# Optimization experiments

Hardware: AMD Instinct MI355X
Metric: run time of the kernel (lower is better)

## Reference

```python
import jax, jax.numpy as jnp
import numpy as np

N = 100000   # nodes
E = 600000   # edges
D_IN, D_H, D_OUT = 128, 128, 128


def glorot(key, shape):
    lim = float(np.sqrt(6.0 / (shape[0] + shape[1])))
    return jax.random.uniform(key, shape, jnp.float32, -lim, lim)


def setup_inputs() -> dict:
    key = jax.random.key(0)
    k1, k2, k3, k4 = jax.random.split(key, 4)
    x = jax.random.normal(k1, (N, D_IN), jnp.float32)
    edge_index = jax.random.randint(k2, (2, E), 0, N, jnp.int64)
    W1 = glorot(k3, (D_IN, D_H))
    b1 = jnp.zeros((D_H,), jnp.float32)
    W2 = glorot(k4, (D_H, D_OUT))
    b2 = jnp.zeros((D_OUT,), jnp.float32)
    return {"x": x, "W1": W1, "b1": b1, "W2": W2, "b2": b2, "edge_index": edge_index}


def gcn_conv(x, W, b, src, dst, n):
    # GCNConv: D^{-1/2}(A+I)D^{-1/2} X W + b  (self loops already in src/dst)
    h = x @ W                                   # [N, d_out]
    ones = jnp.ones(src.shape[0], h.dtype)
    deg = jax.ops.segment_sum(ones, dst, num_segments=n)      # in-degree incl self loop
    dinv = jnp.where(deg > 0, jax.lax.rsqrt(deg), 0.0)        # deg^{-1/2}
    norm = dinv[src] * dinv[dst]                              # [E+N]
    msgs = h[src] * norm[:, None]                             # gather + scale
    out = jax.ops.segment_sum(msgs, dst, num_segments=n)      # scatter-add to targets
    return out + b


def reference(x, W1, b1, W2, b2, edge_index):
    loop = jnp.arange(N, dtype=edge_index.dtype)
    src = jnp.concatenate([edge_index[0], loop])
    dst = jnp.concatenate([edge_index[1], loop])
    h = gcn_conv(x, W1, b1, src, dst, N)
    h = jax.nn.relu(h)  # dropout is a no-op in eval mode
    return gcn_conv(h, W2, b2, src, dst, N)
```

## Files before the change

kernel.cpp:

```cpp
#include <hip/hip_runtime.h>

#define NFEAT 128

typedef __attribute__((ext_vector_type(8))) short bf16x8;
typedef __attribute__((ext_vector_type(4))) float f32x4;

__device__ inline ushort f2b(float v) {
  unsigned u = __builtin_bit_cast(unsigned, v);
  return (ushort)((u + 0x7FFFu + ((u >> 16) & 1u)) >> 16);
}


__global__ __launch_bounds__(256) void k_hist(const int* __restrict__ dst,
                                              int* __restrict__ cnt, int E, int N) {
  int range = blockIdx.x & 7, chunk = blockIdx.x >> 3;
  int lo = (int)(((long long)range * N) >> 3);
  int hi = (int)(((long long)(range + 1) * N) >> 3);
  int i = chunk * 1024 + threadIdx.x * 4;
  if (i + 3 < E) {
    int4 d4 = *(const int4*)(dst + i);
    if ((unsigned)(d4.x - lo) < (unsigned)(hi - lo)) atomicAdd(&cnt[d4.x], 1);
    if ((unsigned)(d4.y - lo) < (unsigned)(hi - lo)) atomicAdd(&cnt[d4.y], 1);
    if ((unsigned)(d4.z - lo) < (unsigned)(hi - lo)) atomicAdd(&cnt[d4.z], 1);
    if ((unsigned)(d4.w - lo) < (unsigned)(hi - lo)) atomicAdd(&cnt[d4.w], 1);
  } else {
    for (int j = 0; j < 4; j++) {
      if (i + j < E) {
        int d = dst[i + j];
        if ((unsigned)(d - lo) < (unsigned)(hi - lo)) atomicAdd(&cnt[d], 1);
      }
    }
  }
}

__global__ __launch_bounds__(256) void k_scan_blocks(const int* __restrict__ cnt,
                                                     int* __restrict__ rowptr,
                                                     int* __restrict__ bsum,
                                                     float* __restrict__ dinv, int n) {
  __shared__ int s[256];
  int tid = threadIdx.x;
  int idx = blockIdx.x * 1024 + tid * 4;
  int v[4];
  int sum = 0;
#pragma unroll
  for (int j = 0; j < 4; j++) {
    int c = 0;
    if (idx + j < n) {
      c = cnt[idx + j];
      dinv[idx + j] = rsqrtf((float)(c + 1));
    }
    v[j] = (idx + j < n) ? ((c + 8) & ~7) : 0;
    sum += v[j];
  }
  s[tid] = sum;
  __syncthreads();
  for (int off = 1; off < 256; off <<= 1) {
    int t = (tid >= off) ? s[tid - off] : 0;
    __syncthreads();
    s[tid] += t;
    __syncthreads();
  }
  if (tid == 255) bsum[blockIdx.x] = s[255];
  int run = s[tid] - sum;
#pragma unroll
  for (int j = 0; j < 4; j++) {
    if (idx + j < n) rowptr[idx + j] = run;
    run += v[j];
  }
}

__global__ __launch_bounds__(256) void k_scan_addcur(int* __restrict__ rowptr,
                                                     const int* __restrict__ bsum,
                                                     int* __restrict__ cursor,
                                                     const float* __restrict__ dinv,
                                                     int2* __restrict__ csr2,
                                                     int n, int nb) {
  __shared__ int s[256];
  int tid = threadIdx.x;
  int v = (tid < nb) ? bsum[tid] : 0;
  s[tid] = v;
  __syncthreads();
  for (int off = 1; off < 256; off <<= 1) {
    int t = (tid >= off) ? s[tid - off] : 0;
    __syncthreads();
    s[tid] += t;
    __syncthreads();
  }
  int total = s[255];
  __syncthreads();
  int ex = s[tid] - v;
  __syncthreads();
  s[tid] = ex;
  __syncthreads();
  int i = blockIdx.x * 256 + tid;
  if (i < n) {
    int rp = rowptr[i] + s[i >> 10];
    rowptr[i] = rp;
    cursor[i] = rp + 1;
    int2 self;
    self.x = i;
    self.y = __float_as_int(dinv[i]);
    csr2[rp] = self;
  }
  if (i == 0) rowptr[n] = total;
}

__global__ __launch_bounds__(256) void k_scatter(const int* __restrict__ src,
                                                 const int* __restrict__ dst,
                                                 const float* __restrict__ dinv,
                                                 int* __restrict__ cursor,
                                                 int2* __restrict__ csr2, int E, int N) {
  int range = blockIdx.x & 7, chunk = blockIdx.x >> 3;
  int lo = (int)(((long long)range * N) >> 3);
  int hi = (int)(((long long)(range + 1) * N) >> 3);
  int i = chunk * 1024 + threadIdx.x * 4;
  if (i + 3 < E) {
    int4 d4 = *(const int4*)(dst + i);
    int4 s4 = *(const int4*)(src + i);
    int dd[4] = {d4.x, d4.y, d4.z, d4.w};
    int ss[4] = {s4.x, s4.y, s4.z, s4.w};
#pragma unroll
    for (int j = 0; j < 4; j++) {
      if ((unsigned)(dd[j] - lo) < (unsigned)(hi - lo)) {
        int p = atomicAdd(&cursor[dd[j]], 1);
        int2 v;
        v.x = ss[j];
        v.y = __float_as_int(dinv[ss[j]]);
        csr2[p] = v;
      }
    }
  } else {
    for (int j = 0; j < 4; j++) {
      if (i + j < E) {
        int d = dst[i + j];
        if ((unsigned)(d - lo) < (unsigned)(hi - lo)) {
          int s = src[i + j];
          int p = atomicAdd(&cursor[d], 1);
          int2 v;
          v.x = s;
          v.y = __float_as_int(dinv[s]);
          csr2[p] = v;
        }
      }
    }
  }
}

__global__ __launch_bounds__(256) void k_cast_w(const float* __restrict__ W1,
                                                const float* __restrict__ W2,
                                                ushort* __restrict__ WT1,
                                                ushort* __restrict__ WT2) {
  int b = blockIdx.x;
  const float* W = (b < 64) ? W1 : W2;
  ushort* WT = (b < 64) ? WT1 : WT2;
  int idx = (b & 63) * 256 + threadIdx.x;
  int k = idx >> 7, nn = idx & 127;
  WT[nn * 128 + k] = f2b(W[idx]);
}


template <bool AFP32>
__global__ __launch_bounds__(256) void k_gemm(const void* __restrict__ Av,
                                              const ushort* __restrict__ WT,
                                              ushort* __restrict__ out, int n) {
  __shared__ ushort sW[128][136];
  int tid = threadIdx.x;
  {
    int r = tid >> 1, hh = tid & 1;
    const uint4* srcp = (const uint4*)(WT + r * 128 + hh * 64);
    uint4* dstp = (uint4*)(&sW[r][hh * 64]);
#pragma unroll
    for (int j = 0; j < 8; j++) dstp[j] = srcp[j];
  }
  __syncthreads();

  int wave = tid >> 6;
  int lane = tid & 63;
  int l16 = lane & 15;
  int quad = lane >> 4;
  int rowBase = blockIdx.x * 128 + wave * 32;

  bf16x8 afrag[2][4];
#pragma unroll
  for (int rt = 0; rt < 2; rt++) {
    int row = rowBase + rt * 16 + l16;
    row = min(row, n - 1);
    if (AFP32) {
      const float* Ap = (const float*)Av + (size_t)row * NFEAT + quad * 8;
#pragma unroll
      for (int ks = 0; ks < 4; ks++) {
        float4 f0 = *(const float4*)(Ap + ks * 32);
        float4 f1 = *(const float4*)(Ap + ks * 32 + 4);
        ushort t[8] = {f2b(f0.x), f2b(f0.y), f2b(f0.z), f2b(f0.w),
                       f2b(f1.x), f2b(f1.y), f2b(f1.z), f2b(f1.w)};
        afrag[rt][ks] = *(const bf16x8*)t;
      }
    } else {
      const ushort* Ap = (const ushort*)Av + (size_t)row * NFEAT + quad * 8;
#pragma unroll
      for (int ks = 0; ks < 4; ks++) afrag[rt][ks] = *(const bf16x8*)(Ap + ks * 32);
    }
  }

#pragma unroll
  for (int ct = 0; ct < 8; ct++) {
    bf16x8 bfrag[4];
#pragma unroll
    for (int ks = 0; ks < 4; ks++)
      bfrag[ks] = *(const bf16x8*)(&sW[ct * 16 + l16][ks * 32 + quad * 8]);
    f32x4 acc[2] = {{0.f, 0.f, 0.f, 0.f}, {0.f, 0.f, 0.f, 0.f}};
#pragma unroll
    for (int rt = 0; rt < 2; rt++)
#pragma unroll
      for (int ks = 0; ks < 4; ks++)
        acc[rt] = __builtin_amdgcn_mfma_f32_16x16x32_bf16(afrag[rt][ks], bfrag[ks],
                                                          acc[rt], 0, 0, 0);
#pragma unroll
    for (int rt = 0; rt < 2; rt++)
#pragma unroll
      for (int r = 0; r < 4; r++) {
        int row = rowBase + rt * 16 + quad * 4 + r;
        if (row < n) out[(size_t)row * NFEAT + ct * 16 + l16] = f2b(acc[rt][r]);
      }
  }
}


__global__ __launch_bounds__(256) void k_agg(const ushort* __restrict__ h,
                                             const float* __restrict__ dinv,
                                             const int* __restrict__ rowptr,
                                             const int2* __restrict__ csr2,
                                             const float* __restrict__ bias,
                                             ushort* __restrict__ out_bf,
                                             float* __restrict__ out_f32,
                                             int n, int relu_bf) {
  int node = blockIdx.x * 8 + (threadIdx.x >> 5);
  if (node >= n) return;
  int c = (threadIdx.x & 31) * 4;
  float a0 = 0.f, a1 = 0.f, a2 = 0.f, a3 = 0.f;

  int e = rowptr[node], end = rowptr[node + 1];
  for (; e < end; e += 8) {
    int4 q0 = *(const int4*)(csr2 + e);
    int4 q1 = *(const int4*)(csr2 + e + 2);
    int4 q2 = *(const int4*)(csr2 + e + 4);
    int4 q3 = *(const int4*)(csr2 + e + 6);
    uint2 h0 = *(const uint2*)(h + (size_t)q0.x * NFEAT + c);
    uint2 h1 = *(const uint2*)(h + (size_t)q0.z * NFEAT + c);
    uint2 h2 = *(const uint2*)(h + (size_t)q1.x * NFEAT + c);
    uint2 h3 = *(const uint2*)(h + (size_t)q1.z * NFEAT + c);
    uint2 h4 = *(const uint2*)(h + (size_t)q2.x * NFEAT + c);
    uint2 h5 = *(const uint2*)(h + (size_t)q2.z * NFEAT + c);
    uint2 h6 = *(const uint2*)(h + (size_t)q3.x * NFEAT + c);
    uint2 h7 = *(const uint2*)(h + (size_t)q3.z * NFEAT + c);
    float w0 = __int_as_float(q0.y), w1 = __int_as_float(q0.w);
    float w2 = __int_as_float(q1.y), w3 = __int_as_float(q1.w);
    float w4 = __int_as_float(q2.y), w5 = __int_as_float(q2.w);
    float w6 = __int_as_float(q3.y), w7 = __int_as_float(q3.w);
    a0 = fmaf(w0, __uint_as_float(h0.x << 16), a0);
    a1 = fmaf(w0, __uint_as_float(h0.x & 0xffff0000u), a1);
    a2 = fmaf(w0, __uint_as_float(h0.y << 16), a2);
    a3 = fmaf(w0, __uint_as_float(h0.y & 0xffff0000u), a3);
    a0 = fmaf(w1, __uint_as_float(h1.x << 16), a0);
    a1 = fmaf(w1, __uint_as_float(h1.x & 0xffff0000u), a1);
    a2 = fmaf(w1, __uint_as_float(h1.y << 16), a2);
    a3 = fmaf(w1, __uint_as_float(h1.y & 0xffff0000u), a3);
    a0 = fmaf(w2, __uint_as_float(h2.x << 16), a0);
    a1 = fmaf(w2, __uint_as_float(h2.x & 0xffff0000u), a1);
    a2 = fmaf(w2, __uint_as_float(h2.y << 16), a2);
    a3 = fmaf(w2, __uint_as_float(h2.y & 0xffff0000u), a3);
    a0 = fmaf(w3, __uint_as_float(h3.x << 16), a0);
    a1 = fmaf(w3, __uint_as_float(h3.x & 0xffff0000u), a1);
    a2 = fmaf(w3, __uint_as_float(h3.y << 16), a2);
    a3 = fmaf(w3, __uint_as_float(h3.y & 0xffff0000u), a3);
    a0 = fmaf(w4, __uint_as_float(h4.x << 16), a0);
    a1 = fmaf(w4, __uint_as_float(h4.x & 0xffff0000u), a1);
    a2 = fmaf(w4, __uint_as_float(h4.y << 16), a2);
    a3 = fmaf(w4, __uint_as_float(h4.y & 0xffff0000u), a3);
    a0 = fmaf(w5, __uint_as_float(h5.x << 16), a0);
    a1 = fmaf(w5, __uint_as_float(h5.x & 0xffff0000u), a1);
    a2 = fmaf(w5, __uint_as_float(h5.y << 16), a2);
    a3 = fmaf(w5, __uint_as_float(h5.y & 0xffff0000u), a3);
    a0 = fmaf(w6, __uint_as_float(h6.x << 16), a0);
    a1 = fmaf(w6, __uint_as_float(h6.x & 0xffff0000u), a1);
    a2 = fmaf(w6, __uint_as_float(h6.y << 16), a2);
    a3 = fmaf(w6, __uint_as_float(h6.y & 0xffff0000u), a3);
    a0 = fmaf(w7, __uint_as_float(h7.x << 16), a0);
    a1 = fmaf(w7, __uint_as_float(h7.x & 0xffff0000u), a1);
    a2 = fmaf(w7, __uint_as_float(h7.y << 16), a2);
    a3 = fmaf(w7, __uint_as_float(h7.y & 0xffff0000u), a3);
  }

  float di = dinv[node];
  float4 b = *(const float4*)(bias + c);
  float o0 = fmaf(di, a0, b.x);
  float o1 = fmaf(di, a1, b.y);
  float o2 = fmaf(di, a2, b.z);
  float o3 = fmaf(di, a3, b.w);
  if (relu_bf) {
    o0 = fmaxf(o0, 0.f); o1 = fmaxf(o1, 0.f);
    o2 = fmaxf(o2, 0.f); o3 = fmaxf(o3, 0.f);
    uint2 pk;
    pk.x = f2b(o0) | ((unsigned)f2b(o1) << 16);
    pk.y = f2b(o2) | ((unsigned)f2b(o3) << 16);
    *(uint2*)(out_bf + (size_t)node * NFEAT + c) = pk;
  } else {
    float4 o = {o0, o1, o2, o3};
    *(float4*)(out_f32 + (size_t)node * NFEAT + c) = o;
  }
}


extern "C" void kernel_launch(void* const* d_in, const int* in_sizes, int n_in,
                              void* d_out, int out_size, void* d_ws, size_t ws_size,
                              hipStream_t stream) {
  const float* x = (const float*)d_in[0];
  const float* W1 = (const float*)d_in[1];
  const float* b1 = (const float*)d_in[2];
  const float* W2 = (const float*)d_in[3];
  const float* b2 = (const float*)d_in[4];
  const int* ei = (const int*)d_in[5];

  const int N = in_sizes[0] / NFEAT;
  const int E = in_sizes[5] / 2;
  const int* srcIdx = ei;
  const int* dstIdx = ei + E;

  char* p = (char*)d_ws;
  auto alloc = [&](size_t bytes) {
    char* r = p;
    p += (bytes + 255) & ~(size_t)255;
    return r;
  };
  int* cnt = (int*)alloc((size_t)N * 4);
  int2* csr2 = (int2*)alloc((size_t)(E + 8 * N + 16) * 8);
  char* memset_end = p;
  int* cursor = (int*)alloc((size_t)N * 4);
  float* dinv = (float*)alloc((size_t)N * 4);
  int* rowptr = (int*)alloc((size_t)(N + 1) * 4);
  int* bsum = (int*)alloc(1024);
  ushort* WT1 = (ushort*)alloc(NFEAT * NFEAT * 2);
  ushort* WT2 = (ushort*)alloc(NFEAT * NFEAT * 2);
  ushort* t1 = (ushort*)alloc((size_t)N * NFEAT * 2);
  ushort* h2 = (ushort*)alloc((size_t)N * NFEAT * 2);
  ushort* h1 = (ushort*)d_out;
  float* out = (float*)d_out;

  hipMemsetAsync(cnt, 0, (size_t)(memset_end - (char*)cnt), stream);

  int nb = (N + 1023) / 1024;
  int gEx = ((E + 1023) / 1024) * 8;

  k_hist<<<gEx, 256, 0, stream>>>(dstIdx, cnt, E, N);
  k_scan_blocks<<<nb, 256, 0, stream>>>(cnt, rowptr, bsum, dinv, N);
  k_scan_addcur<<<(N + 255) / 256, 256, 0, stream>>>(rowptr, bsum, cursor, dinv, csr2,
                                                     N, nb);
  k_scatter<<<gEx, 256, 0, stream>>>(srcIdx, dstIdx, dinv, cursor, csr2, E, N);
  k_cast_w<<<128, 256, 0, stream>>>(W1, W2, WT1, WT2);

  int gG = (N + 127) / 128;
  int gA = (N + 7) / 8;

  k_gemm<true><<<gG, 256, 0, stream>>>(x, WT1, h1, N);
  k_agg<<<gA, 256, 0, stream>>>(h1, dinv, rowptr, csr2, b1, t1, nullptr, N, 1);
  k_gemm<false><<<gG, 256, 0, stream>>>(t1, WT2, h2, N);
  k_agg<<<gA, 256, 0, stream>>>(h2, dinv, rowptr, csr2, b2, nullptr, out, N, 0);
}
```

Measured before the change: 265.9 us.

## Fuse layer-1 aggregation with layer-2 GEMM and overlap histogram with first GEMM

Several restructurings land together. The first GEMM and the in-degree histogram now run as one launch, with blocks split between the two roles. The first-layer aggregation (with bias and ReLU) is fused with the second GEMM through shared memory, so the t1 intermediate is no longer written to and read back from global memory. CSR row padding drops from 8 to 4, with the gather loop unrolled 4-wide to match, and scan_addcur blocks are remapped by node range, probably for locality with the scatter partitioning. The risks are less memory-level parallelism in the gather loop, and lower occupancy in the fused kernel from its larger shared-memory footprint and serial per-block aggregation batches.

```diff
diff --git a/kernel.cpp b/kernel.cpp
--- a/kernel.cpp
+++ b/kernel.cpp
@@ -10,253 +10,18 @@
   return (ushort)((u + 0x7FFFu + ((u >> 16) & 1u)) >> 16);
 }
 
-
-__global__ __launch_bounds__(256) void k_hist(const int* __restrict__ dst,
-                                              int* __restrict__ cnt, int E, int N) {
-  int range = blockIdx.x & 7, chunk = blockIdx.x >> 3;
-  int lo = (int)(((long long)range * N) >> 3);
-  int hi = (int)(((long long)(range + 1) * N) >> 3);
-  int i = chunk * 1024 + threadIdx.x * 4;
-  if (i + 3 < E) {
-    int4 d4 = *(const int4*)(dst + i);
-    if ((unsigned)(d4.x - lo) < (unsigned)(hi - lo)) atomicAdd(&cnt[d4.x], 1);
-    if ((unsigned)(d4.y - lo) < (unsigned)(hi - lo)) atomicAdd(&cnt[d4.y], 1);
-    if ((unsigned)(d4.z - lo) < (unsigned)(hi - lo)) atomicAdd(&cnt[d4.z], 1);
-    if ((unsigned)(d4.w - lo) < (unsigned)(hi - lo)) atomicAdd(&cnt[d4.w], 1);
-  } else {
-    for (int j = 0; j < 4; j++) {
-      if (i + j < E) {
-        int d = dst[i + j];
-        if ((unsigned)(d - lo) < (unsigned)(hi - lo)) atomicAdd(&cnt[d], 1);
-      }
-    }
-  }
-}
-
-__global__ __launch_bounds__(256) void k_scan_blocks(const int* __restrict__ cnt,
-                                                     int* __restrict__ rowptr,
-                                                     int* __restrict__ bsum,
-                                                     float* __restrict__ dinv, int n) {
-  __shared__ int s[256];
-  int tid = threadIdx.x;
-  int idx = blockIdx.x * 1024 + tid * 4;
-  int v[4];
-  int sum = 0;
-#pragma unroll
-  for (int j = 0; j < 4; j++) {
-    int c = 0;
-    if (idx + j < n) {
-      c = cnt[idx + j];
-      dinv[idx + j] = rsqrtf((float)(c + 1));
-    }
-    v[j] = (idx + j < n) ? ((c + 8) & ~7) : 0;
-    sum += v[j];
-  }
-  s[tid] = sum;
-  __syncthreads();
-  for (int off = 1; off < 256; off <<= 1) {
-    int t = (tid >= off) ? s[tid - off] : 0;
-    __syncthreads();
-    s[tid] += t;
-    __syncthreads();
-  }
-  if (tid == 255) bsum[blockIdx.x] = s[255];
-  int run = s[tid] - sum;
-#pragma unroll
-  for (int j = 0; j < 4; j++) {
-    if (idx + j < n) rowptr[idx + j] = run;
-    run += v[j];
-  }
-}
-
-__global__ __launch_bounds__(256) void k_scan_addcur(int* __restrict__ rowptr,
-                                                     const int* __restrict__ bsum,
-                                                     int* __restrict__ cursor,
-                                                     const float* __restrict__ dinv,
-                                                     int2* __restrict__ csr2,
-                                                     int n, int nb) {
-  __shared__ int s[256];
-  int tid = threadIdx.x;
-  int v = (tid < nb) ? bsum[tid] : 0;
-  s[tid] = v;
-  __syncthreads();
-  for (int off = 1; off < 256; off <<= 1) {
-    int t = (tid >= off) ? s[tid - off] : 0;
-    __syncthreads();
-    s[tid] += t;
-    __syncthreads();
-  }
-  int total = s[255];
-  __syncthreads();
-  int ex = s[tid] - v;
-  __syncthreads();
-  s[tid] = ex;
-  __syncthreads();
-  int i = blockIdx.x * 256 + tid;
-  if (i < n) {
-    int rp = rowptr[i] + s[i >> 10];
-    rowptr[i] = rp;
-    cursor[i] = rp + 1;
-    int2 self;
-    self.x = i;
-    self.y = __float_as_int(dinv[i]);
-    csr2[rp] = self;
-  }
-  if (i == 0) rowptr[n] = total;
-}
-
-__global__ __launch_bounds__(256) void k_scatter(const int* __restrict__ src,
-                                                 const int* __restrict__ dst,
-                                                 const float* __restrict__ dinv,
-                                                 int* __restrict__ cursor,
-                                                 int2* __restrict__ csr2, int E, int N) {
-  int range = blockIdx.x & 7, chunk = blockIdx.x >> 3;
-  int lo = (int)(((long long)range * N) >> 3);
-  int hi = (int)(((long long)(range + 1) * N) >> 3);
-  int i = chunk * 1024 + threadIdx.x * 4;
-  if (i + 3 < E) {
-    int4 d4 = *(const int4*)(dst + i);
-    int4 s4 = *(const int4*)(src + i);
-    int dd[4] = {d4.x, d4.y, d4.z, d4.w};
-    int ss[4] = {s4.x, s4.y, s4.z, s4.w};
-#pragma unroll
-    for (int j = 0; j < 4; j++) {
-      if ((unsigned)(dd[j] - lo) < (unsigned)(hi - lo)) {
-        int p = atomicAdd(&cursor[dd[j]], 1);
-        int2 v;
-        v.x = ss[j];
-        v.y = __float_as_int(dinv[ss[j]]);
-        csr2[p] = v;
-      }
-    }
-  } else {
-    for (int j = 0; j < 4; j++) {
-      if (i + j < E) {
-        int d = dst[i + j];
-        if ((unsigned)(d - lo) < (unsigned)(hi - lo)) {
-          int s = src[i + j];
-          int p = atomicAdd(&cursor[d], 1);
-          int2 v;
-          v.x = s;
-          v.y = __float_as_int(dinv[s]);
-          csr2[p] = v;
-        }
-      }
-    }
-  }
-}
-
-__global__ __launch_bounds__(256) void k_cast_w(const float* __restrict__ W1,
-                                                const float* __restrict__ W2,
-                                                ushort* __restrict__ WT1,
-                                                ushort* __restrict__ WT2) {
-  int b = blockIdx.x;
-  const float* W = (b < 64) ? W1 : W2;
-  ushort* WT = (b < 64) ? WT1 : WT2;
-  int idx = (b & 63) * 256 + threadIdx.x;
-  int k = idx >> 7, nn = idx & 127;
-  WT[nn * 128 + k] = f2b(W[idx]);
-}
-
-
-template <bool AFP32>
-__global__ __launch_bounds__(256) void k_gemm(const void* __restrict__ Av,
-                                              const ushort* __restrict__ WT,
-                                              ushort* __restrict__ out, int n) {
-  __shared__ ushort sW[128][136];
-  int tid = threadIdx.x;
-  {
-    int r = tid >> 1, hh = tid & 1;
-    const uint4* srcp = (const uint4*)(WT + r * 128 + hh * 64);
-    uint4* dstp = (uint4*)(&sW[r][hh * 64]);
-#pragma unroll
-    for (int j = 0; j < 8; j++) dstp[j] = srcp[j];
-  }
-  __syncthreads();
-
-  int wave = tid >> 6;
-  int lane = tid & 63;
-  int l16 = lane & 15;
-  int quad = lane >> 4;
-  int rowBase = blockIdx.x * 128 + wave * 32;
-
-  bf16x8 afrag[2][4];
-#pragma unroll
-  for (int rt = 0; rt < 2; rt++) {
-    int row = rowBase + rt * 16 + l16;
-    row = min(row, n - 1);
-    if (AFP32) {
-      const float* Ap = (const float*)Av + (size_t)row * NFEAT + quad * 8;
-#pragma unroll
-      for (int ks = 0; ks < 4; ks++) {
-        float4 f0 = *(const float4*)(Ap + ks * 32);
-        float4 f1 = *(const float4*)(Ap + ks * 32 + 4);
-        ushort t[8] = {f2b(f0.x), f2b(f0.y), f2b(f0.z), f2b(f0.w),
-                       f2b(f1.x), f2b(f1.y), f2b(f1.z), f2b(f1.w)};
-        afrag[rt][ks] = *(const bf16x8*)t;
-      }
-    } else {
-      const ushort* Ap = (const ushort*)Av + (size_t)row * NFEAT + quad * 8;
-#pragma unroll
-      for (int ks = 0; ks < 4; ks++) afrag[rt][ks] = *(const bf16x8*)(Ap + ks * 32);
-    }
-  }
-
-#pragma unroll
-  for (int ct = 0; ct < 8; ct++) {
-    bf16x8 bfrag[4];
-#pragma unroll
-    for (int ks = 0; ks < 4; ks++)
-      bfrag[ks] = *(const bf16x8*)(&sW[ct * 16 + l16][ks * 32 + quad * 8]);
-    f32x4 acc[2] = {{0.f, 0.f, 0.f, 0.f}, {0.f, 0.f, 0.f, 0.f}};
-#pragma unroll
-    for (int rt = 0; rt < 2; rt++)
-#pragma unroll
-      for (int ks = 0; ks < 4; ks++)
-        acc[rt] = __builtin_amdgcn_mfma_f32_16x16x32_bf16(afrag[rt][ks], bfrag[ks],
-                                                          acc[rt], 0, 0, 0);
-#pragma unroll
-    for (int rt = 0; rt < 2; rt++)
-#pragma unroll
-      for (int r = 0; r < 4; r++) {
-        int row = rowBase + rt * 16 + quad * 4 + r;
-        if (row < n) out[(size_t)row * NFEAT + ct * 16 + l16] = f2b(acc[rt][r]);
-      }
-  }
-}
-
-
-__global__ __launch_bounds__(256) void k_agg(const ushort* __restrict__ h,
-                                             const float* __restrict__ dinv,
-                                             const int* __restrict__ rowptr,
-                                             const int2* __restrict__ csr2,
-                                             const float* __restrict__ bias,
-                                             ushort* __restrict__ out_bf,
-                                             float* __restrict__ out_f32,
-                                             int n, int relu_bf) {
-  int node = blockIdx.x * 8 + (threadIdx.x >> 5);
-  if (node >= n) return;
-  int c = (threadIdx.x & 31) * 4;
-  float a0 = 0.f, a1 = 0.f, a2 = 0.f, a3 = 0.f;
-
-  int e = rowptr[node], end = rowptr[node + 1];
-  for (; e < end; e += 8) {
+__device__ inline void agg_accum(const ushort* __restrict__ h,
+                                 const int2* __restrict__ csr2, int e, int end, int c,
+                                 float& a0, float& a1, float& a2, float& a3) {
+  for (; e < end; e += 4) {
     int4 q0 = *(const int4*)(csr2 + e);
     int4 q1 = *(const int4*)(csr2 + e + 2);
-    int4 q2 = *(const int4*)(csr2 + e + 4);
-    int4 q3 = *(const int4*)(csr2 + e + 6);
     uint2 h0 = *(const uint2*)(h + (size_t)q0.x * NFEAT + c);
     uint2 h1 = *(const uint2*)(h + (size_t)q0.z * NFEAT + c);
     uint2 h2 = *(const uint2*)(h + (size_t)q1.x * NFEAT + c);
     uint2 h3 = *(const uint2*)(h + (size_t)q1.z * NFEAT + c);
-    uint2 h4 = *(const uint2*)(h + (size_t)q2.x * NFEAT + c);
-    uint2 h5 = *(const uint2*)(h + (size_t)q2.z * NFEAT + c);
-    uint2 h6 = *(const uint2*)(h + (size_t)q3.x * NFEAT + c);
-    uint2 h7 = *(const uint2*)(h + (size_t)q3.z * NFEAT + c);
     float w0 = __int_as_float(q0.y), w1 = __int_as_float(q0.w);
     float w2 = __int_as_float(q1.y), w3 = __int_as_float(q1.w);
-    float w4 = __int_as_float(q2.y), w5 = __int_as_float(q2.w);
-    float w6 = __int_as_float(q3.y), w7 = __int_as_float(q3.w);
     a0 = fmaf(w0, __uint_as_float(h0.x << 16), a0);
     a1 = fmaf(w0, __uint_as_float(h0.x & 0xffff0000u), a1);
     a2 = fmaf(w0, __uint_as_float(h0.y << 16), a2);
@@ -273,41 +38,311 @@
     a1 = fmaf(w3, __uint_as_float(h3.x & 0xffff0000u), a1);
     a2 = fmaf(w3, __uint_as_float(h3.y << 16), a2);
     a3 = fmaf(w3, __uint_as_float(h3.y & 0xffff0000u), a3);
-    a0 = fmaf(w4, __uint_as_float(h4.x << 16), a0);
-    a1 = fmaf(w4, __uint_as_float(h4.x & 0xffff0000u), a1);
-    a2 = fmaf(w4, __uint_as_float(h4.y << 16), a2);
-    a3 = fmaf(w4, __uint_as_float(h4.y & 0xffff0000u), a3);
-    a0 = fmaf(w5, __uint_as_float(h5.x << 16), a0);
-    a1 = fmaf(w5, __uint_as_float(h5.x & 0xffff0000u), a1);
-    a2 = fmaf(w5, __uint_as_float(h5.y << 16), a2);
-    a3 = fmaf(w5, __uint_as_float(h5.y & 0xffff0000u), a3);
-    a0 = fmaf(w6, __uint_as_float(h6.x << 16), a0);
-    a1 = fmaf(w6, __uint_as_float(h6.x & 0xffff0000u), a1);
-    a2 = fmaf(w6, __uint_as_float(h6.y << 16), a2);
-    a3 = fmaf(w6, __uint_as_float(h6.y & 0xffff0000u), a3);
-    a0 = fmaf(w7, __uint_as_float(h7.x << 16), a0);
-    a1 = fmaf(w7, __uint_as_float(h7.x & 0xffff0000u), a1);
-    a2 = fmaf(w7, __uint_as_float(h7.y << 16), a2);
-    a3 = fmaf(w7, __uint_as_float(h7.y & 0xffff0000u), a3);
-  }
-
+  }
+}
+
+__global__ __launch_bounds__(256) void k_cast_w(const float* __restrict__ W1,
+                                                const float* __restrict__ W2,
+                                                ushort* __restrict__ WT1,
+                                                ushort* __restrict__ WT2) {
+  int b = blockIdx.x;
+  const float* W = (b < 64) ? W1 : W2;
+  ushort* WT = (b < 64) ? WT1 : WT2;
+  int idx = (b & 63) * 256 + threadIdx.x;
+  int k = idx >> 7, nn = idx & 127;
+  WT[nn * 128 + k] = f2b(W[idx]);
+}
+
+
+__global__ __launch_bounds__(256) void k_par1(const float* __restrict__ x,
+                                              const ushort* __restrict__ WT1,
+                                              ushort* __restrict__ h1, int n,
+                                              const int* __restrict__ dst,
+                                              int* __restrict__ cnt, int E,
+                                              int gemmBlocks) {
+  if ((int)blockIdx.x >= gemmBlocks) {
+    int bid = blockIdx.x - gemmBlocks;
+    int range = bid & 7, chunk = bid >> 3;
+    int lo = (int)(((long long)range * n) >> 3);
+    int hi = (int)(((long long)(range + 1) * n) >> 3);
+    int i = chunk * 1024 + threadIdx.x * 4;
+    if (i + 3 < E) {
+      int4 d4 = *(const int4*)(dst + i);
+      if ((unsigned)(d4.x - lo) < (unsigned)(hi - lo)) atomicAdd(&cnt[d4.x], 1);
+      if ((unsigned)(d4.y - lo) < (unsigned)(hi - lo)) atomicAdd(&cnt[d4.y], 1);
+      if ((unsigned)(d4.z - lo) < (unsigned)(hi - lo)) atomicAdd(&cnt[d4.z], 1);
+      if ((unsigned)(d4.w - lo) < (unsigned)(hi - lo)) atomicAdd(&cnt[d4.w], 1);
+    } else {
+      for (int j = 0; j < 4; j++) {
+        if (i + j < E) {
+          int d = dst[i + j];
+          if ((unsigned)(d - lo) < (unsigned)(hi - lo)) atomicAdd(&cnt[d], 1);
+        }
+      }
+    }
+    return;
+  }
+  __shared__ ushort sW[128][136];
+  int tid = threadIdx.x;
+  {
+    int r = tid >> 1, hh = tid & 1;
+    const uint4* srcp = (const uint4*)(WT1 + r * 128 + hh * 64);
+    uint4* dstp = (uint4*)(&sW[r][hh * 64]);
+#pragma unroll
+    for (int j = 0; j < 8; j++) dstp[j] = srcp[j];
+  }
+  __syncthreads();
+
+  int wave = tid >> 6;
+  int lane = tid & 63;
+  int l16 = lane & 15;
+  int quad = lane >> 4;
+  int rowBase = blockIdx.x * 128 + wave * 32;
+
+  bf16x8 afrag[2][4];
+#pragma unroll
+  for (int rt = 0; rt < 2; rt++) {
+    int row = rowBase + rt * 16 + l16;
+    row = min(row, n - 1);
+    const float* Ap = x + (size_t)row * NFEAT + quad * 8;
+#pragma unroll
+    for (int ks = 0; ks < 4; ks++) {
+      float4 f0 = *(const float4*)(Ap + ks * 32);
+      float4 f1 = *(const float4*)(Ap + ks * 32 + 4);
+      ushort t[8] = {f2b(f0.x), f2b(f0.y), f2b(f0.z), f2b(f0.w),
+                     f2b(f1.x), f2b(f1.y), f2b(f1.z), f2b(f1.w)};
+      afrag[rt][ks] = *(const bf16x8*)t;
+    }
+  }
+
+#pragma unroll
+  for (int ct = 0; ct < 8; ct++) {
+    bf16x8 bfrag[4];
+#pragma unroll
+    for (int ks = 0; ks < 4; ks++)
+      bfrag[ks] = *(const bf16x8*)(&sW[ct * 16 + l16][ks * 32 + quad * 8]);
+    f32x4 acc[2] = {{0.f, 0.f, 0.f, 0.f}, {0.f, 0.f, 0.f, 0.f}};
+#pragma unroll
+    for (int rt = 0; rt < 2; rt++)
+#pragma unroll
+      for (int ks = 0; ks < 4; ks++)
+        acc[rt] = __builtin_amdgcn_mfma_f32_16x16x32_bf16(afrag[rt][ks], bfrag[ks],
+                                                          acc[rt], 0, 0, 0);
+#pragma unroll
+    for (int rt = 0; rt < 2; rt++)
+#pragma unroll
+      for (int r = 0; r < 4; r++) {
+        int row = rowBase + rt * 16 + quad * 4 + r;
+        if (row < n) h1[(size_t)row * NFEAT + ct * 16 + l16] = f2b(acc[rt][r]);
+      }
+  }
+}
+
+__global__ __launch_bounds__(256) void k_scan_blocks(const int* __restrict__ cnt,
+                                                     int* __restrict__ rowptr,
+                                                     int* __restrict__ bsum,
+                                                     float* __restrict__ dinv, int n) {
+  __shared__ int s[256];
+  int tid = threadIdx.x;
+  int idx = blockIdx.x * 1024 + tid * 4;
+  int v[4];
+  int sum = 0;
+#pragma unroll
+  for (int j = 0; j < 4; j++) {
+    int c = 0;
+    if (idx + j < n) {
+      c = cnt[idx + j];
+      dinv[idx + j] = rsqrtf((float)(c + 1));
+    }
+    v[j] = (idx + j < n) ? ((c + 4) & ~3) : 0;
+    sum += v[j];
+  }
+  s[tid] = sum;
+  __syncthreads();
+  for (int off = 1; off < 256; off <<= 1) {
+    int t = (tid >= off) ? s[tid - off] : 0;
+    __syncthreads();
+    s[tid] += t;
+    __syncthreads();
+  }
+  if (tid == 255) bsum[blockIdx.x] = s[255];
+  int run = s[tid] - sum;
+#pragma unroll
+  for (int j = 0; j < 4; j++) {
+    if (idx + j < n) rowptr[idx + j] = run;
+    run += v[j];
+  }
+}
+
+__global__ __launch_bounds__(256) void k_scan_addcur(int* __restrict__ rowptr,
+                                                     const int* __restrict__ bsum,
+                                                     int* __restrict__ cursor,
+                                                     const float* __restrict__ dinv,
+                                                     int2* __restrict__ csr2,
+                                                     int n, int nb) {
+  __shared__ int s[256];
+  int tid = threadIdx.x;
+  int v = (tid < nb) ? bsum[tid] : 0;
+  s[tid] = v;
+  __syncthreads();
+  for (int off = 1; off < 256; off <<= 1) {
+    int t = (tid >= off) ? s[tid - off] : 0;
+    __syncthreads();
+    s[tid] += t;
+    __syncthreads();
+  }
+  int total = s[255];
+  __syncthreads();
+  int ex = s[tid] - v;
+  __syncthreads();
+  s[tid] = ex;
+  __syncthreads();
+  int range = blockIdx.x & 7, chunk = blockIdx.x >> 3;
+  int lo = (int)(((long long)range * n) >> 3);
+  int hi = (int)(((long long)(range + 1) * n) >> 3);
+  int i = lo + chunk * 256 + tid;
+  if (i < hi) {
+    int rp = rowptr[i] + s[i >> 10];
+    rowptr[i] = rp;
+    cursor[i] = rp + 1;
+    int2 self;
+    self.x = i;
+    self.y = __float_as_int(dinv[i]);
+    csr2[rp] = self;
+  }
+  if (blockIdx.x == 0 && tid == 0) rowptr[n] = total;
+}
+
+__global__ __launch_bounds__(256) void k_scatter(const int* __restrict__ src,
+                                                 const int* __restrict__ dst,
+                                                 const float* __restrict__ dinv,
+                                                 int* __restrict__ cursor,
+                                                 int2* __restrict__ csr2, int E, int N) {
+  int range = blockIdx.x & 7, chunk = blockIdx.x >> 3;
+  int lo = (int)(((long long)range * N) >> 3);
+  int hi = (int)(((long long)(range + 1) * N) >> 3);
+  int i = chunk * 1024 + threadIdx.x * 4;
+  if (i + 3 < E) {
+    int4 d4 = *(const int4*)(dst + i);
+    int4 s4 = *(const int4*)(src + i);
+    int dd[4] = {d4.x, d4.y, d4.z, d4.w};
+    int ss[4] = {s4.x, s4.y, s4.z, s4.w};
+#pragma unroll
+    for (int j = 0; j < 4; j++) {
+      if ((unsigned)(dd[j] - lo) < (unsigned)(hi - lo)) {
+        int p = atomicAdd(&cursor[dd[j]], 1);
+        int2 v;
+        v.x = ss[j];
+        v.y = __float_as_int(dinv[ss[j]]);
+        csr2[p] = v;
+      }
+    }
+  } else {
+    for (int j = 0; j < 4; j++) {
+      if (i + j < E) {
+        int d = dst[i + j];
+        if ((unsigned)(d - lo) < (unsigned)(hi - lo)) {
+          int s = src[i + j];
+          int p = atomicAdd(&cursor[d], 1);
+          int2 v;
+          v.x = s;
+          v.y = __float_as_int(dinv[s]);
+          csr2[p] = v;
+        }
+      }
+    }
+  }
+}
+
+
+__global__ __launch_bounds__(256) void k_fused(const ushort* __restrict__ h1,
+                                               const float* __restrict__ dinv,
+                                               const int* __restrict__ rowptr,
+                                               const int2* __restrict__ csr2,
+                                               const float* __restrict__ b1,
+                                               const ushort* __restrict__ WT2,
+                                               ushort* __restrict__ h2, int n) {
+  __shared__ ushort sW[128][136];
+  __shared__ ushort sT[64][136];
+  int tid = threadIdx.x;
+  {
+    int r = tid >> 1, hh = tid & 1;
+    const uint4* srcp = (const uint4*)(WT2 + r * 128 + hh * 64);
+    uint4* dstp = (uint4*)(&sW[r][hh * 64]);
+#pragma unroll
+    for (int j = 0; j < 8; j++) dstp[j] = srcp[j];
+  }
+
+  int base = blockIdx.x * 64;
+  int c = (tid & 31) * 4;
+#pragma unroll 1
+  for (int batch = 0; batch < 8; batch++) {
+    int nl = batch * 8 + (tid >> 5);
+    int node = base + nl;
+    if (node < n) {
+      float a0 = 0.f, a1 = 0.f, a2 = 0.f, a3 = 0.f;
+      agg_accum(h1, csr2, rowptr[node], rowptr[node + 1], c, a0, a1, a2, a3);
+      float di = dinv[node];
+      float4 bb = *(const float4*)(b1 + c);
+      float o0 = fmaxf(fmaf(di, a0, bb.x), 0.f);
+      float o1 = fmaxf(fmaf(di, a1, bb.y), 0.f);
+      float o2 = fmaxf(fmaf(di, a2, bb.z), 0.f);
+      float o3 = fmaxf(fmaf(di, a3, bb.w), 0.f);
+      uint2 pk;
+      pk.x = f2b(o0) | ((unsigned)f2b(o1) << 16);
+      pk.y = f2b(o2) | ((unsigned)f2b(o3) << 16);
+      *(uint2*)(&sT[nl][c]) = pk;
+    }
+  }
+  __syncthreads();
+
+  int wave = tid >> 6;
+  int lane = tid & 63;
+  int l16 = lane & 15;
+  int quad = lane >> 4;
+  bf16x8 afrag[4];
+#pragma unroll
+  for (int ks = 0; ks < 4; ks++)
+    afrag[ks] = *(const bf16x8*)(&sT[wave * 16 + l16][ks * 32 + quad * 8]);
+
+#pragma unroll
+  for (int ct = 0; ct < 8; ct++) {
+    bf16x8 bfrag[4];
+#pragma unroll
+    for (int ks = 0; ks < 4; ks++)
+      bfrag[ks] = *(const bf16x8*)(&sW[ct * 16 + l16][ks * 32 + quad * 8]);
+    f32x4 acc = {0.f, 0.f, 0.f, 0.f};
+#pragma unroll
+    for (int ks = 0; ks < 4; ks++)
+      acc = __builtin_amdgcn_mfma_f32_16x16x32_bf16(afrag[ks], bfrag[ks], acc, 0, 0, 0);
+#pragma unroll
+    for (int r = 0; r < 4; r++) {
+      int row = base + wave * 16 + quad * 4 + r;
+      if (row < n) h2[(size_t)row * NFEAT + ct * 16 + l16] = f2b(acc[r]);
+    }
+  }
+}
+
+
+__global__ __launch_bounds__(256) void k_agg2(const ushort* __restrict__ h,
+                                              const float* __restrict__ dinv,
+                                              const int* __restrict__ rowptr,
+                                              const int2* __restrict__ csr2,
+                                              const float* __restrict__ bias,
+                                              float* __restrict__ out, int n) {
+  int node = blockIdx.x * 8 + (threadIdx.x >> 5);
+  if (node >= n) return;
+  int c = (threadIdx.x & 31) * 4;
+  float a0 = 0.f, a1 = 0.f, a2 = 0.f, a3 = 0.f;
+  agg_accum(h, csr2, rowptr[node], rowptr[node + 1], c, a0, a1, a2, a3);
   float di = dinv[node];
   float4 b = *(const float4*)(bias + c);
-  float o0 = fmaf(di, a0, b.x);
-  float o1 = fmaf(di, a1, b.y);
-  float o2 = fmaf(di, a2, b.z);
-  float o3 = fmaf(di, a3, b.w);
-  if (relu_bf) {
-    o0 = fmaxf(o0, 0.f); o1 = fmaxf(o1, 0.f);
-    o2 = fmaxf(o2, 0.f); o3 = fmaxf(o3, 0.f);
-    uint2 pk;
-    pk.x = f2b(o0) | ((unsigned)f2b(o1) << 16);
-    pk.y = f2b(o2) | ((unsigned)f2b(o3) << 16);
-    *(uint2*)(out_bf + (size_t)node * NFEAT + c) = pk;
-  } else {
-    float4 o = {o0, o1, o2, o3};
-    *(float4*)(out_f32 + (size_t)node * NFEAT + c) = o;
-  }
+  float4 o;
+  o.x = fmaf(di, a0, b.x);
+  o.y = fmaf(di, a1, b.y);
+  o.z = fmaf(di, a2, b.z);
+  o.w = fmaf(di, a3, b.w);
+  *(float4*)(out + (size_t)node * NFEAT + c) = o;
 }
 
 
@@ -333,7 +368,7 @@
     return r;
   };
   int* cnt = (int*)alloc((size_t)N * 4);
-  int2* csr2 = (int2*)alloc((size_t)(E + 8 * N + 16) * 8);
+  int2* csr2 = (int2*)alloc((size_t)(E + 4 * N + 16) * 8);
   char* memset_end = p;
   int* cursor = (int*)alloc((size_t)N * 4);
   float* dinv = (float*)alloc((size_t)N * 4);
@@ -341,7 +376,6 @@
   int* bsum = (int*)alloc(1024);
   ushort* WT1 = (ushort*)alloc(NFEAT * NFEAT * 2);
   ushort* WT2 = (ushort*)alloc(NFEAT * NFEAT * 2);
-  ushort* t1 = (ushort*)alloc((size_t)N * NFEAT * 2);
   ushort* h2 = (ushort*)alloc((size_t)N * NFEAT * 2);
   ushort* h1 = (ushort*)d_out;
   float* out = (float*)d_out;
@@ -350,19 +384,14 @@
 
   int nb = (N + 1023) / 1024;
   int gEx = ((E + 1023) / 1024) * 8;
-
-  k_hist<<<gEx, 256, 0, stream>>>(dstIdx, cnt, E, N);
+  int gG1 = (N + 127) / 128;
+  int cpr = (((N + 7) / 8) + 255) / 256;
+
+  k_cast_w<<<128, 256, 0, stream>>>(W1, W2, WT1, WT2);
+  k_par1<<<gG1 + gEx, 256, 0, stream>>>(x, WT1, h1, N, dstIdx, cnt, E, gG1);
   k_scan_blocks<<<nb, 256, 0, stream>>>(cnt, rowptr, bsum, dinv, N);
-  k_scan_addcur<<<(N + 255) / 256, 256, 0, stream>>>(rowptr, bsum, cursor, dinv, csr2,
-                                                     N, nb);
+  k_scan_addcur<<<8 * cpr, 256, 0, stream>>>(rowptr, bsum, cursor, dinv, csr2, N, nb);
   k_scatter<<<gEx, 256, 0, stream>>>(srcIdx, dstIdx, dinv, cursor, csr2, E, N);
-  k_cast_w<<<128, 256, 0, stream>>>(W1, W2, WT1, WT2);
-
-  int gG = (N + 127) / 128;
-  int gA = (N + 7) / 8;
-
-  k_gemm<true><<<gG, 256, 0, stream>>>(x, WT1, h1, N);
-  k_agg<<<gA, 256, 0, stream>>>(h1, dinv, rowptr, csr2, b1, t1, nullptr, N, 1);
-  k_gemm<false><<<gG, 256, 0, stream>>>(t1, WT2, h2, N);
-  k_agg<<<gA, 256, 0, stream>>>(h2, dinv, rowptr, csr2, b2, nullptr, out, N, 0);
-}
+  k_fused<<<(N + 63) / 64, 256, 0, stream>>>(h1, dinv, rowptr, csr2, b1, WT2, h2, N);
+  k_agg2<<<(N + 7) / 8, 256, 0, stream>>>(h2, dinv, rowptr, csr2, b2, out, N);
+}
```

Measured after the change: 276.4 us. 1.04x slower.
